# Optimization experiments

Measured on AMD Instinct MI355X. Metric: run time of the kernel, lower is better.

The kernel has to match this reference:

```python
import jax, jax.numpy as jnp
import numpy as np


def gru_layer(x, W_ih, W_hh, b_ih, b_hh):
    """PyTorch-semantics GRU over a full sequence.
    x: [B, T, F]; W_ih: [3H, F]; W_hh: [3H, H]; biases: [3H].
    Gate order (r, z, n) per torch.nn.GRU. Returns [B, T, H].
    """
    B, T, _ = x.shape
    H = W_hh.shape[1]
    # Precompute input projections for all timesteps as one big GEMM: [B, T, 3H]
    xg = jnp.einsum('btf,gf->btg', x, W_ih) + b_ih

    def step(h, xg_t):
        gh = h @ W_hh.T + b_hh                      # [B, 3H]
        xr, xz, xn = jnp.split(xg_t, 3, axis=-1)
        hr, hz, hn = jnp.split(gh, 3, axis=-1)
        r = jax.nn.sigmoid(xr + hr)
        z = jax.nn.sigmoid(xz + hz)
        n = jnp.tanh(xn + r * hn)
        h_new = (1.0 - z) * n + z * h
        return h_new, h_new

    h0 = jnp.zeros((B, H), dtype=x.dtype)
    _, hs = jax.lax.scan(step, h0, jnp.swapaxes(xg, 0, 1))  # hs: [T, B, H]
    return jnp.swapaxes(hs, 0, 1)


def setup_inputs() -> dict:
    key = jax.random.key(0)
    ks = jax.random.split(key, 16)
    B, T, F = 512, 256, 64
    H1, H2, H3 = 256, 128, 64

    def w(k, shape, fan_in):
        s = 1.0 / np.sqrt(fan_in)
        return jax.random.uniform(k, shape, jnp.float32, -s, s)

    return {
        'x': jax.random.normal(ks[0], (B, T, F), jnp.float32),
        'W_ih1': w(ks[1], (3 * H1, F), H1),
        'W_hh1': w(ks[2], (3 * H1, H1), H1),
        'b_ih1': w(ks[3], (3 * H1,), H1),
        'b_hh1': w(ks[4], (3 * H1,), H1),
        'W_ih2': w(ks[5], (3 * H2, H1), H2),
        'W_hh2': w(ks[6], (3 * H2, H2), H2),
        'b_ih2': w(ks[7], (3 * H2,), H2),
        'b_hh2': w(ks[8], (3 * H2,), H2),
        'W_ih3': w(ks[9], (3 * H3, H2), H3),
        'W_hh3': w(ks[10], (3 * H3, H3), H3),
        'b_ih3': w(ks[11], (3 * H3,), H3),
        'b_hh3': w(ks[12], (3 * H3,), H3),
        'W_dense': w(ks[13], (1, H3), H3),
        'b_dense': w(ks[14], (1,), H3),
    }


def reference(x, W_ih1, W_hh1, b_ih1, b_hh1,
              W_ih2, W_hh2, b_ih2, b_hh2,
              W_ih3, W_hh3, b_ih3, b_hh3,
              W_dense, b_dense):
    # Dropout layers act as identity in eval mode.
    h = gru_layer(x, W_ih1, W_hh1, b_ih1, b_hh1)   # [B, T, 256]
    h = gru_layer(h, W_ih2, W_hh2, b_ih2, b_hh2)   # [B, T, 128]
    h = gru_layer(h, W_ih3, W_hh3, b_ih3, b_hh3)   # [B, T, 64]
    last = h[:, -1, :]                              # [B, 64]
    return last @ W_dense.T + b_dense               # [B, 1]
```

## Files before the change

### kernel.cpp

```cpp
#include <hip/hip_runtime.h>
#include <cstddef>

typedef _Float16 f16x8 __attribute__((ext_vector_type(8)));
typedef _Float16 f16x4 __attribute__((ext_vector_type(4)));
typedef short    s16x8 __attribute__((ext_vector_type(8)));
typedef short    s16x4 __attribute__((ext_vector_type(4)));
typedef float    f32x4 __attribute__((ext_vector_type(4)));

#define MFMA_F16(a, b, c) __builtin_amdgcn_mfma_f32_16x16x32_f16((a), (b), (c), 0, 0, 0)

constexpr int GB = 512, GT = 256, GF = 64;
constexpr int H1 = 256, H2 = 128, H3 = 64;

#if __has_builtin(__builtin_amdgcn_rcpf)
__device__ __forceinline__ float fast_rcp(float x) { return __builtin_amdgcn_rcpf(x); }
#else
__device__ __forceinline__ float fast_rcp(float x) { return 1.f / x; }
#endif

__device__ __forceinline__ f16x8 ld8(const short* p) {
  return __builtin_bit_cast(f16x8, *(const s16x8*)p);
}
__device__ __forceinline__ f16x4 ld4(const short* p) {
  return __builtin_bit_cast(f16x4, *(const s16x4*)p);
}

__device__ __forceinline__ void barrier_nodrain() {
  asm volatile("s_waitcnt lgkmcnt(0)" ::: "memory");
  __builtin_amdgcn_s_barrier();
  asm volatile("" ::: "memory");
}

struct CastDesc { const float* src; short* dst; int n; };
struct CastArgs {
  CastDesc d[7];
  const float* bih2; const float* bhh2; float* bc2;
};

__global__ void cast_many(CastArgs a) {
  const int tid = blockIdx.x * blockDim.x + threadIdx.x;
  const int stride = gridDim.x * blockDim.x;
#pragma unroll
  for (int j = 0; j < 7; j++) {
    const float* __restrict__ s = a.d[j].src;
    short* __restrict__ o = a.d[j].dst;
    const int n = a.d[j].n;
    for (int i = tid; i < n; i += stride)
      o[i] = __builtin_bit_cast(short, (_Float16)s[i]);
  }
  for (int i = tid; i < 3 * H2; i += stride)
    a.bc2[i] = a.bih2[i] + (i < 2 * H2 ? a.bhh2[i] : 0.f);
}

template <int K, int NO, int JT>
__device__ __forceinline__ void g_body(const short* __restrict__ A,
                                       const short* __restrict__ W,
                                       const float* __restrict__ biasC,
                                       short* __restrict__ slot, int TC,
                                       int bt, int trel, int tabs, int tid) {
  constexpr int KC = K / 32;
  constexpr int TT = 16;
  const int lane = tid & 63, wid = tid >> 6;
  const int p = lane & 15, q = lane >> 4;
  const int j0 = wid * 16 * JT;

  f16x8 wb[JT][KC];
  float bc[JT];
#pragma unroll
  for (int jt = 0; jt < JT; jt++) {
    const int col = j0 + jt * 16 + p;
    bc[jt] = biasC[col];
#pragma unroll
    for (int kc = 0; kc < KC; kc++)
      wb[jt][kc] = ld8(W + (size_t)col * K + kc * 32 + q * 8);
  }
  const short* arow = A + ((size_t)(bt * 16 + p) * GT + tabs) * K + q * 8;
  short* outb = slot + ((size_t)bt * TC + trel) * NO * 16;

  f16x8 a0[KC], a1[KC];
#pragma unroll
  for (int kc = 0; kc < KC; kc++) a0[kc] = ld8(arow + kc * 32);

  auto step = [&](int ti, f16x8 (&ac)[KC], f16x8 (&anx)[KC], bool pf) {
    if (pf) {
#pragma unroll
      for (int kc = 0; kc < KC; kc++)
        anx[kc] = ld8(arow + (size_t)(ti + 1) * K + kc * 32);
    }
    f32x4 acc[JT];
#pragma unroll
    for (int jt = 0; jt < JT; jt++)
      acc[jt] = f32x4{bc[jt], bc[jt], bc[jt], bc[jt]};
#pragma unroll
    for (int kc = 0; kc < KC; kc++)
#pragma unroll
      for (int jt = 0; jt < JT; jt++)
        acc[jt] = MFMA_F16(ac[kc], wb[jt][kc], acc[jt]);
    short* ob = outb + (size_t)ti * NO * 16;
#pragma unroll
    for (int jt = 0; jt < JT; jt++) {
      const int col = j0 + jt * 16 + p;
      s16x4 v;
#pragma unroll
      for (int r = 0; r < 4; r++)
        v[r] = __builtin_bit_cast(short, (_Float16)acc[jt][r]);
      *(s16x4*)&ob[col * 16 + q * 4] = v;
    }
  };

#pragma unroll 1
  for (int ti = 0; ti < TT; ti += 2) {
    step(ti, a0, a1, true);
    step(ti + 1, a1, a0, ti + 2 < TT);
  }
}

template <int K, int NO, int JT>
__global__ __launch_bounds__(512, 2)
void g_kern(const short* __restrict__ A, const short* __restrict__ W,
            const float* __restrict__ biasC, short* __restrict__ slot,
            int TC, int tbase) {
  const int nty = TC / 16;
  const int bt = blockIdx.x / nty, ty = blockIdx.x - bt * nty;
  g_body<K, NO, JT>(A, W, biasC, slot, TC, bt, ty * 16, tbase + ty * 16, threadIdx.x);
}

__device__ __forceinline__ void r1_run(const short* __restrict__ xg,
                                       const short* __restrict__ Whh,
                                       const float* __restrict__ bhh,
                                       short* __restrict__ hseq,
                                       float* __restrict__ hstate,
                                       int bt, int t0, int t1, int TC,
                                       short* smem, int tid) {
  constexpr int H = H1, KS = H / 32, JT = 2;
  constexpr int HP = H + 8, NO = 3 * H;

  short* wn = smem;
  short* hb = smem + H * HP;

  const int lane = tid & 63, wid = tid >> 6;
  const int p = lane & 15, q = lane >> 4;
  const int b0 = bt * 16, j0 = wid * 16 * JT;

  {
    constexpr int KV = H / 8;
    for (int i = tid; i < H * KV; i += 512) {
      const int row = i / KV, kc = i - row * KV;
      *(s16x8*)&wn[row * HP + kc * 8] =
          *(const s16x8*)&Whh[(size_t)(2 * H + row) * H + kc * 8];
    }
  }
  if (t0 == 0) {
    for (int i = tid; i < 16 * HP; i += 512) hb[i] = 0;
  } else {
    for (int i = tid; i < 16 * H; i += 512) {
      const int row = i / H, col = i - row * H;
      hb[row * HP + col] =
          __builtin_bit_cast(short, (_Float16)hstate[(size_t)(b0 + row) * H + col]);
    }
  }

  f16x8 wr[JT][2][KS];
#pragma unroll
  for (int jt = 0; jt < JT; jt++) {
    const int col = j0 + jt * 16 + p;
#pragma unroll
    for (int g = 0; g < 2; g++)
#pragma unroll
      for (int k = 0; k < KS; k++)
        wr[jt][g][k] = ld8(Whh + (size_t)(g * H + col) * H + k * 32 + q * 8);
  }
  float bhr[JT], bhz[JT], bhn[JT];
  int wrow[JT];
#pragma unroll
  for (int jt = 0; jt < JT; jt++) {
    const int col = j0 + jt * 16 + p;
    wrow[jt] = col;
    bhr[jt] = bhh[col];
    bhz[jt] = bhh[H + col];
    bhn[jt] = bhh[2 * H + col];
  }

  float hprev[JT][4];
#pragma unroll
  for (int jt = 0; jt < JT; jt++)
#pragma unroll
    for (int r = 0; r < 4; r++)
      hprev[jt][r] = (t0 == 0) ? 0.f
                   : hstate[(size_t)(b0 + q * 4 + r) * H + (j0 + jt * 16 + p)];

  const size_t sbase = (size_t)bt * TC * NO * 16;
  int loff[JT][3];
#pragma unroll
  for (int jt = 0; jt < JT; jt++)
#pragma unroll
    for (int g = 0; g < 3; g++)
      loff[jt][g] = (g * H + j0 + jt * 16 + p) * 16 + q * 4;

  f16x4 xb[2][JT][3];
#pragma unroll
  for (int u = 0; u < 2; u++)
#pragma unroll
    for (int jt = 0; jt < JT; jt++)
#pragma unroll
      for (int g = 0; g < 3; g++)
        xb[u][jt][g] = ld4(xg + sbase + (size_t)u * NO * 16 + loff[jt][g]);

  __syncthreads();

  const int steps = t1 - t0;
#pragma unroll 1
  for (int sb = 0; sb < steps; sb += 2) {
#pragma unroll
    for (int u = 0; u < 2; u++) {
      const int s = sb + u, t = t0 + s;
      short* hbc = hb + u * 16 * HP;
      short* hbn = hb + (u ^ 1) * 16 * HP;

      f32x4 ar[JT], az[JT], an[JT];
#pragma unroll
      for (int jt = 0; jt < JT; jt++) {
#pragma unroll
        for (int r = 0; r < 4; r++) {
          ar[jt][r] = (float)xb[u][jt][0][r];
          az[jt][r] = (float)xb[u][jt][1][r];
        }
        an[jt] = f32x4{0.f, 0.f, 0.f, 0.f};
      }
#pragma unroll
      for (int k = 0; k < KS; k++) {
        const f16x8 ahk = ld8(&hbc[p * HP + k * 32 + q * 8]);
#pragma unroll
        for (int jt = 0; jt < JT; jt++) {
          ar[jt] = MFMA_F16(ahk, wr[jt][0][k], ar[jt]);
          az[jt] = MFMA_F16(ahk, wr[jt][1][k], az[jt]);
          const f16x8 wnk = ld8(&wn[wrow[jt] * HP + k * 32 + q * 8]);
          an[jt] = MFMA_F16(ahk, wnk, an[jt]);
        }
      }
#pragma unroll
      for (int jt = 0; jt < JT; jt++) {
        const int col = j0 + jt * 16 + p;
#pragma unroll
        for (int r = 0; r < 4; r++) {
          const int bm = q * 4 + r;
          const float rpre = ar[jt][r] + bhr[jt];
          const float zpre = az[jt][r] + bhz[jt];
          const float rg = fast_rcp(1.f + __expf(-rpre));
          const float zg = fast_rcp(1.f + __expf(-zpre));
          const float narg = (float)xb[u][jt][2][r] + rg * (an[jt][r] + bhn[jt]);
          const float e2 = __expf(2.f * narg);
          const float ng = 1.f - 2.f * fast_rcp(e2 + 1.f);
          const float hnew = (1.f - zg) * ng + zg * hprev[jt][r];
          hprev[jt][r] = hnew;
          const _Float16 hf = (_Float16)hnew;
          hbn[bm * HP + col] = __builtin_bit_cast(short, hf);
          hseq[((size_t)(b0 + bm) * GT + t) * H + col] = __builtin_bit_cast(short, hf);
        }
      }
      if (t == t1 - 1) {
#pragma unroll
        for (int jt = 0; jt < JT; jt++)
#pragma unroll
          for (int r = 0; r < 4; r++)
            hstate[(size_t)(b0 + q * 4 + r) * H + (j0 + jt * 16 + p)] = hprev[jt][r];
      }
      {
        const size_t s2 = sbase + (size_t)(s + 2) * NO * 16;
#pragma unroll
        for (int jt = 0; jt < JT; jt++)
#pragma unroll
          for (int g = 0; g < 3; g++)
            xb[u][jt][g] = ld4(xg + s2 + loff[jt][g]);
      }
      barrier_nodrain();
    }
  }
}

__device__ __forceinline__ void rec23_run(const short* __restrict__ xg2,
                                          const short* __restrict__ Whh2,
                                          const float* __restrict__ bhh2,
                                          const short* __restrict__ Wih3,
                                          const short* __restrict__ Whh3,
                                          const float* __restrict__ bih3,
                                          const float* __restrict__ bhh3,
                                          float* __restrict__ hs2,
                                          float* __restrict__ hs3,
                                          int bt, int t0, int t1, int TC,
                                          short* smem, int tid) {
  constexpr int HP2 = H2 + 8, HP3 = H3 + 8, NO = 3 * H2;
  short* hb2 = smem;
  short* hb3 = smem + 2 * 16 * HP2;

  const int lane = tid & 63, wid = tid >> 6;
  const int p = lane & 15, q = lane >> 4;
  const int b0 = bt * 16;
  const int col2 = wid * 16 + p;
  const int col3 = (wid & 3) * 16 + p;
  const bool act3 = wid < 4;

  if (t0 == 0) {
    for (int i = tid; i < 2 * 16 * HP2; i += 512) hb2[i] = 0;
    for (int i = tid; i < 2 * 16 * HP3; i += 512) hb3[i] = 0;
  } else {
    for (int i = tid; i < 16 * H2; i += 512) {
      const int r = i / H2, c = i - r * H2;
      hb2[r * HP2 + c] = __builtin_bit_cast(short, (_Float16)hs2[(size_t)(b0 + r) * H2 + c]);
    }
    for (int i = tid; i < 16 * H3; i += 512) {
      const int r = i / H3, c = i - r * H3;
      hb3[r * HP3 + c] = __builtin_bit_cast(short, (_Float16)hs3[(size_t)(b0 + r) * H3 + c]);
    }
  }

  f16x8 w2[3][4];
#pragma unroll
  for (int g = 0; g < 3; g++)
#pragma unroll
    for (int k = 0; k < 4; k++)
      w2[g][k] = ld8(Whh2 + (size_t)(g * H2 + col2) * H2 + k * 32 + q * 8);
  const float bn2 = bhh2[2 * H2 + col2];

  f16x8 wi3[3][4], wh3[3][2];
  float br3 = 0.f, bz3 = 0.f, bn3x = 0.f, bn3h = 0.f;
  if (act3) {
#pragma unroll
    for (int g = 0; g < 3; g++) {
#pragma unroll
      for (int k = 0; k < 4; k++)
        wi3[g][k] = ld8(Wih3 + (size_t)(g * H3 + col3) * H2 + k * 32 + q * 8);
#pragma unroll
      for (int k = 0; k < 2; k++)
        wh3[g][k] = ld8(Whh3 + (size_t)(g * H3 + col3) * H3 + k * 32 + q * 8);
    }
    br3 = bih3[col3] + bhh3[col3];
    bz3 = bih3[H3 + col3] + bhh3[H3 + col3];
    bn3x = bih3[2 * H3 + col3];
    bn3h = bhh3[2 * H3 + col3];
  }

  float h2p[4], h3p[4];
#pragma unroll
  for (int r = 0; r < 4; r++) {
    h2p[r] = (t0 == 0) ? 0.f : hs2[(size_t)(b0 + q * 4 + r) * H2 + col2];
    h3p[r] = (!act3 || t0 == 0) ? 0.f : hs3[(size_t)(b0 + q * 4 + r) * H3 + col3];
  }

  const size_t sbase = (size_t)bt * TC * NO * 16;
  int loff[3];
#pragma unroll
  for (int g = 0; g < 3; g++) loff[g] = (g * H2 + col2) * 16 + q * 4;
  f16x4 xb[2][3];
#pragma unroll
  for (int u = 0; u < 2; u++)
#pragma unroll
    for (int g = 0; g < 3; g++)
      xb[u][g] = ld4(xg2 + sbase + (size_t)u * NO * 16 + loff[g]);

  __syncthreads();

  const int steps = t1 - t0;
#pragma unroll 1
  for (int sb = 0; sb < steps; sb += 2) {
#pragma unroll
    for (int u = 0; u < 2; ++u) {
      const int s = sb + u, t = t0 + s;
      f32x4 ar, az, an;
#pragma unroll
      for (int r = 0; r < 4; r++) { ar[r] = (float)xb[u][0][r]; az[r] = (float)xb[u][1][r]; }
      an = f32x4{0.f, 0.f, 0.f, 0.f};
#pragma unroll
      for (int k = 0; k < 4; k++) {
        const f16x8 ahk = ld8(&hb2[(u * 16 + p) * HP2 + k * 32 + q * 8]);
        ar = MFMA_F16(ahk, w2[0][k], ar);
        az = MFMA_F16(ahk, w2[1][k], az);
        an = MFMA_F16(ahk, w2[2][k], an);
      }
#pragma unroll
      for (int r = 0; r < 4; r++) {
        const int bm = q * 4 + r;
        const float rg = fast_rcp(1.f + __expf(-ar[r]));
        const float zg = fast_rcp(1.f + __expf(-az[r]));
        const float narg = (float)xb[u][2][r] + rg * (an[r] + bn2);
        const float e2 = __expf(2.f * narg);
        const float ng = 1.f - 2.f * fast_rcp(e2 + 1.f);
        const float hnew = (1.f - zg) * ng + zg * h2p[r];
        h2p[r] = hnew;
        hb2[((u ^ 1) * 16 + bm) * HP2 + col2] = __builtin_bit_cast(short, (_Float16)hnew);
        if (t == t1 - 1) hs2[(size_t)(b0 + bm) * H2 + col2] = hnew;
      }
      {
        const size_t s2 = sbase + (size_t)(s + 2) * NO * 16;
#pragma unroll
        for (int g = 0; g < 3; g++) xb[u][g] = ld4(xg2 + s2 + loff[g]);
      }
      barrier_nodrain();
      if (act3) {
        f32x4 a3r{0.f,0.f,0.f,0.f}, a3z{0.f,0.f,0.f,0.f},
              a3x{0.f,0.f,0.f,0.f}, a3h{0.f,0.f,0.f,0.f};
#pragma unroll
        for (int k = 0; k < 4; k++) {
          const f16x8 a2k = ld8(&hb2[((u ^ 1) * 16 + p) * HP2 + k * 32 + q * 8]);
          a3r = MFMA_F16(a2k, wi3[0][k], a3r);
          a3z = MFMA_F16(a2k, wi3[1][k], a3z);
          a3x = MFMA_F16(a2k, wi3[2][k], a3x);
        }
#pragma unroll
        for (int k = 0; k < 2; k++) {
          const f16x8 a3k = ld8(&hb3[(u * 16 + p) * HP3 + k * 32 + q * 8]);
          a3r = MFMA_F16(a3k, wh3[0][k], a3r);
          a3z = MFMA_F16(a3k, wh3[1][k], a3z);
          a3h = MFMA_F16(a3k, wh3[2][k], a3h);
        }
#pragma unroll
        for (int r = 0; r < 4; r++) {
          const int bm = q * 4 + r;
          const float rg = fast_rcp(1.f + __expf(-(a3r[r] + br3)));
          const float zg = fast_rcp(1.f + __expf(-(a3z[r] + bz3)));
          const float narg = a3x[r] + bn3x + rg * (a3h[r] + bn3h);
          const float e2 = __expf(2.f * narg);
          const float ng = 1.f - 2.f * fast_rcp(e2 + 1.f);
          const float hnew = (1.f - zg) * ng + zg * h3p[r];
          h3p[r] = hnew;
          hb3[((u ^ 1) * 16 + bm) * HP3 + col3] = __builtin_bit_cast(short, (_Float16)hnew);
          if (t == t1 - 1) hs3[(size_t)(b0 + bm) * H3 + col3] = hnew;
        }
      }
    }
  }
}

__global__ __launch_bounds__(512, 2)
void fused1(const short* __restrict__ xg_rd, short* __restrict__ xg_wr,
            const short* __restrict__ xh, const short* __restrict__ wih1,
            const float* __restrict__ bih1, const short* __restrict__ whh1,
            const float* __restrict__ bhh1, short* __restrict__ h1,
            float* __restrict__ hs1, int t0, int TC) {
  extern __shared__ __align__(16) short smem[];
  if (blockIdx.x < 32) {
    r1_run(xg_rd, whh1, bhh1, h1, hs1, blockIdx.x, t0, t0 + TC, TC, smem, threadIdx.x);
  } else if (xg_wr) {
    const int g = blockIdx.x - 32, nty = TC / 16;
    const int bt = g / nty, ty = g - bt * nty;
    g_body<GF, 3 * H1, 6>(xh, wih1, bih1, xg_wr, TC, bt, ty * 16,
                          t0 + TC + ty * 16, threadIdx.x);
  }
}

__global__ __launch_bounds__(512, 2)
void fused2(const short* __restrict__ xg_rd, short* __restrict__ xg_wr,
            const short* __restrict__ h1, const short* __restrict__ wih2,
            const float* __restrict__ bc2, const short* __restrict__ whh2,
            const float* __restrict__ bhh2, const short* __restrict__ wih3,
            const short* __restrict__ whh3, const float* __restrict__ bih3,
            const float* __restrict__ bhh3, float* __restrict__ hs2,
            float* __restrict__ hs3, int t0, int TC) {
  extern __shared__ __align__(16) short smem[];
  if (blockIdx.x < 32) {
    rec23_run(xg_rd, whh2, bhh2, wih3, whh3, bih3, bhh3, hs2, hs3,
              blockIdx.x, t0, t0 + TC, TC, smem, threadIdx.x);
  } else if (xg_wr) {
    const int g = blockIdx.x - 32, nty = TC / 16;
    const int bt = g / nty, ty = g - bt * nty;
    g_body<H1, 3 * H2, 3>(h1, wih2, bc2, xg_wr, TC, bt, ty * 16,
                          t0 + TC + ty * 16, threadIdx.x);
  }
}

__global__ void dense_kernel(const float* __restrict__ hl, const float* __restrict__ Wd,
                             const float* __restrict__ bd, float* __restrict__ out) {
  const int b = blockIdx.x * 64 + threadIdx.x;
  float a = bd[0];
#pragma unroll
  for (int k = 0; k < 64; k++) a = fmaf(hl[b * 64 + k], Wd[k], a);
  out[b] = a;
}

extern "C" void kernel_launch(void* const* d_in, const int* in_sizes, int n_in,
                              void* d_out, int out_size, void* d_ws, size_t ws_size,
                              hipStream_t stream) {
  constexpr int B = GB, T = GT, F = GF;
  constexpr int M = B * T;

  const float* x     = (const float*)d_in[0];
  const float* W_ih1 = (const float*)d_in[1];
  const float* W_hh1 = (const float*)d_in[2];
  const float* b_ih1 = (const float*)d_in[3];
  const float* b_hh1 = (const float*)d_in[4];
  const float* W_ih2 = (const float*)d_in[5];
  const float* W_hh2 = (const float*)d_in[6];
  const float* b_ih2 = (const float*)d_in[7];
  const float* b_hh2 = (const float*)d_in[8];
  const float* W_ih3 = (const float*)d_in[9];
  const float* W_hh3 = (const float*)d_in[10];
  const float* b_ih3 = (const float*)d_in[11];
  const float* b_hh3 = (const float*)d_in[12];
  const float* W_d   = (const float*)d_in[13];
  const float* b_d   = (const float*)d_in[14];
  float* out = (float*)d_out;

  char* ws = (char*)d_ws;
  size_t off = 0;
  auto alloc = [&](size_t bytes) -> char* {
    char* pp = ws + off;
    off = (off + bytes + 255) & ~(size_t)255;
    return pp;
  };

  const int nx    = M * F;
  const int nwih1 = 3 * H1 * F,  nwhh1 = 3 * H1 * H1;
  const int nwih2 = 3 * H2 * H1, nwhh2 = 3 * H2 * H2;
  const int nwih3 = 3 * H3 * H2, nwhh3 = 3 * H3 * H3;

  short* xh   = (short*)alloc((size_t)nx * 2);
  short* wih1 = (short*)alloc((size_t)nwih1 * 2);
  short* whh1 = (short*)alloc((size_t)nwhh1 * 2);
  short* wih2 = (short*)alloc((size_t)nwih2 * 2);
  short* whh2 = (short*)alloc((size_t)nwhh2 * 2);
  short* wih3 = (short*)alloc((size_t)nwih3 * 2);
  short* whh3 = (short*)alloc((size_t)nwhh3 * 2);
  short* h1   = (short*)alloc((size_t)M * H1 * 2);
  float* hs1  = (float*)alloc((size_t)B * H1 * 4);
  float* hs2  = (float*)alloc((size_t)B * H2 * 4);
  float* hs3  = (float*)alloc((size_t)B * H3 * 4);
  float* bc2  = (float*)alloc(3 * H2 * 4);
  (void)n_in; (void)in_sizes; (void)out_size;

  const size_t avail = (ws_size > off) ? (ws_size - off) : 0;
  int TC = 64;
  auto need = [&](int tc) -> size_t {
    return 2 * ((size_t)32 * tc * (3 * H1) * 16 * 2)
         + 2 * ((size_t)32 * tc * (3 * H2) * 16 * 2) + 2 * 65536;
  };
  while (TC > 16 && need(TC) > avail) TC >>= 1;
  const int NC = T / TC, nty = TC / 16;
  const size_t slot1e = (size_t)32 * TC * (3 * H1) * 16;
  const size_t slot2e = (size_t)32 * TC * (3 * H2) * 16;
  short* ring1 = (short*)alloc(2 * slot1e * 2 + 65536);
  short* ring2 = (short*)alloc(2 * slot2e * 2 + 65536);

  CastArgs ca;
  ca.d[0] = {x, xh, nx};
  ca.d[1] = {W_ih1, wih1, nwih1};
  ca.d[2] = {W_hh1, whh1, nwhh1};
  ca.d[3] = {W_ih2, wih2, nwih2};
  ca.d[4] = {W_hh2, whh2, nwhh2};
  ca.d[5] = {W_ih3, wih3, nwih3};
  ca.d[6] = {W_hh3, whh3, nwhh3};
  ca.bih2 = b_ih2; ca.bhh2 = b_hh2; ca.bc2 = bc2;
  cast_many<<<1024, 256, 0, stream>>>(ca);

  constexpr int SM1 = H1 * (H1 + 8) * 2 + 2 * 16 * (H1 + 8) * 2;
  constexpr int SM2 = 2 * 16 * (H2 + 8) * 2 + 2 * 16 * (H3 + 8) * 2;
  (void)hipFuncSetAttribute((const void*)fused1,
                            hipFuncAttributeMaxDynamicSharedMemorySize, SM1);

  g_kern<GF, 3 * H1, 6><<<32 * nty, 512, 0, stream>>>(xh, wih1, b_ih1, ring1, TC, 0);
  for (int c = 0; c < NC; ++c) {
    const short* rd = ring1 + (size_t)(c & 1) * slot1e;
    short* wr = (c + 1 < NC) ? ring1 + (size_t)((c + 1) & 1) * slot1e : nullptr;
    fused1<<<32 + (wr ? 32 * nty : 0), 512, SM1, stream>>>(
        rd, wr, xh, wih1, b_ih1, whh1, b_hh1, h1, hs1, c * TC, TC);
  }
  g_kern<H1, 3 * H2, 3><<<32 * nty, 512, 0, stream>>>(h1, wih2, bc2, ring2, TC, 0);
  for (int c = 0; c < NC; ++c) {
    const short* rd = ring2 + (size_t)(c & 1) * slot2e;
    short* wr = (c + 1 < NC) ? ring2 + (size_t)((c + 1) & 1) * slot2e : nullptr;
    fused2<<<32 + (wr ? 32 * nty : 0), 512, SM2, stream>>>(
        rd, wr, h1, wih2, bc2, whh2, b_hh2, wih3, whh3, b_ih3, b_hh3,
        hs2, hs3, c * TC, TC);
  }

  dense_kernel<<<B / 64, 64, 0, stream>>>(hs3, W_d, b_d, out);
}
```

Measured before the change: 940.0 us.

## Wavefront-pipeline layer-1 and layer-2/3 recurrences across time chunks in one kernel

Merges the two per-layer chunk loops into a single launch sequence. Each launch runs the layer-1 recurrence on chunk c and the fused layer-2/3 recurrence on chunk c-2 at the same time. In the same launch, other blocks compute the layer-1 input projection for chunk c+1 and the layer-2 input projection for chunk c-1. This lets the two serial recurrences overlap instead of running back to back, and removes the separate layer-2 prologue GEMM. In exchange every block requests the larger layer-1 shared-memory size, which may lower occupancy. The recurrence blocks also now share the GPU with more concurrent work.

```diff
diff --git a/kernel.cpp b/kernel.cpp
--- a/kernel.cpp
+++ b/kernel.cpp
@@ -431,40 +431,48 @@
   }
 }
 
+struct PipeArgs {
+  const short* xh;
+  const short* wih1; const short* whh1; const float* bih1; const float* bhh1;
+  const short* wih2; const float* bc2;  const short* whh2; const float* bhh2;
+  const short* wih3; const short* whh3; const float* bih3; const float* bhh3;
+  short* h1; float* hs1; float* hs2; float* hs3;
+  short* ring1; short* ring2;
+  size_t slot1e, slot2e;
+  int c, NC, TC;
+};
+
 __global__ __launch_bounds__(512, 2)
-void fused1(const short* __restrict__ xg_rd, short* __restrict__ xg_wr,
-            const short* __restrict__ xh, const short* __restrict__ wih1,
-            const float* __restrict__ bih1, const short* __restrict__ whh1,
-            const float* __restrict__ bhh1, short* __restrict__ h1,
-            float* __restrict__ hs1, int t0, int TC) {
+void fused_all(PipeArgs a) {
   extern __shared__ __align__(16) short smem[];
-  if (blockIdx.x < 32) {
-    r1_run(xg_rd, whh1, bhh1, h1, hs1, blockIdx.x, t0, t0 + TC, TC, smem, threadIdx.x);
-  } else if (xg_wr) {
-    const int g = blockIdx.x - 32, nty = TC / 16;
-    const int bt = g / nty, ty = g - bt * nty;
-    g_body<GF, 3 * H1, 6>(xh, wih1, bih1, xg_wr, TC, bt, ty * 16,
-                          t0 + TC + ty * 16, threadIdx.x);
-  }
-}
-
-__global__ __launch_bounds__(512, 2)
-void fused2(const short* __restrict__ xg_rd, short* __restrict__ xg_wr,
-            const short* __restrict__ h1, const short* __restrict__ wih2,
-            const float* __restrict__ bc2, const short* __restrict__ whh2,
-            const float* __restrict__ bhh2, const short* __restrict__ wih3,
-            const short* __restrict__ whh3, const float* __restrict__ bih3,
-            const float* __restrict__ bhh3, float* __restrict__ hs2,
-            float* __restrict__ hs3, int t0, int TC) {
-  extern __shared__ __align__(16) short smem[];
-  if (blockIdx.x < 32) {
-    rec23_run(xg_rd, whh2, bhh2, wih3, whh3, bih3, bhh3, hs2, hs3,
-              blockIdx.x, t0, t0 + TC, TC, smem, threadIdx.x);
-  } else if (xg_wr) {
-    const int g = blockIdx.x - 32, nty = TC / 16;
-    const int bt = g / nty, ty = g - bt * nty;
-    g_body<H1, 3 * H2, 3>(h1, wih2, bc2, xg_wr, TC, bt, ty * 16,
-                          t0 + TC + ty * 16, threadIdx.x);
+  const int nty = a.TC / 16, GW = 32 * nty;
+  const int bid = blockIdx.x, tid = threadIdx.x;
+  if (bid < 32) {
+    if (a.c < a.NC)
+      r1_run(a.ring1 + (size_t)(a.c & 1) * a.slot1e, a.whh1, a.bhh1, a.h1, a.hs1,
+             bid, a.c * a.TC, (a.c + 1) * a.TC, a.TC, smem, tid);
+  } else if (bid < 64) {
+    const int cc = a.c - 2;
+    if (cc >= 0 && cc < a.NC)
+      rec23_run(a.ring2 + (size_t)(cc & 1) * a.slot2e, a.whh2, a.bhh2,
+                a.wih3, a.whh3, a.bih3, a.bhh3, a.hs2, a.hs3,
+                bid - 32, cc * a.TC, (cc + 1) * a.TC, a.TC, smem, tid);
+  } else if (bid < 64 + GW) {
+    const int cc = a.c + 1;
+    if (cc < a.NC) {
+      const int g = bid - 64, bt = g / nty, ty = g - bt * nty;
+      g_body<GF, 3 * H1, 6>(a.xh, a.wih1, a.bih1,
+                            a.ring1 + (size_t)(cc & 1) * a.slot1e, a.TC,
+                            bt, ty * 16, cc * a.TC + ty * 16, tid);
+    }
+  } else {
+    const int cc = a.c - 1;
+    if (cc >= 0 && cc < a.NC) {
+      const int g = bid - 64 - GW, bt = g / nty, ty = g - bt * nty;
+      g_body<H1, 3 * H2, 3>(a.h1, a.wih2, a.bc2,
+                            a.ring2 + (size_t)(cc & 1) * a.slot2e, a.TC,
+                            bt, ty * 16, cc * a.TC + ty * 16, tid);
+    }
   }
 }
 
@@ -552,24 +560,25 @@
   cast_many<<<1024, 256, 0, stream>>>(ca);
 
   constexpr int SM1 = H1 * (H1 + 8) * 2 + 2 * 16 * (H1 + 8) * 2;
-  constexpr int SM2 = 2 * 16 * (H2 + 8) * 2 + 2 * 16 * (H3 + 8) * 2;
-  (void)hipFuncSetAttribute((const void*)fused1,
+  (void)hipFuncSetAttribute((const void*)fused_all,
                             hipFuncAttributeMaxDynamicSharedMemorySize, SM1);
 
   g_kern<GF, 3 * H1, 6><<<32 * nty, 512, 0, stream>>>(xh, wih1, b_ih1, ring1, TC, 0);
-  for (int c = 0; c < NC; ++c) {
-    const short* rd = ring1 + (size_t)(c & 1) * slot1e;
-    short* wr = (c + 1 < NC) ? ring1 + (size_t)((c + 1) & 1) * slot1e : nullptr;
-    fused1<<<32 + (wr ? 32 * nty : 0), 512, SM1, stream>>>(
-        rd, wr, xh, wih1, b_ih1, whh1, b_hh1, h1, hs1, c * TC, TC);
-  }
-  g_kern<H1, 3 * H2, 3><<<32 * nty, 512, 0, stream>>>(h1, wih2, bc2, ring2, TC, 0);
-  for (int c = 0; c < NC; ++c) {
-    const short* rd = ring2 + (size_t)(c & 1) * slot2e;
-    short* wr = (c + 1 < NC) ? ring2 + (size_t)((c + 1) & 1) * slot2e : nullptr;
-    fused2<<<32 + (wr ? 32 * nty : 0), 512, SM2, stream>>>(
-        rd, wr, h1, wih2, bc2, whh2, b_hh2, wih3, whh3, b_ih3, b_hh3,
-        hs2, hs3, c * TC, TC);
+
+  PipeArgs pa;
+  pa.xh = xh;
+  pa.wih1 = wih1; pa.whh1 = whh1; pa.bih1 = b_ih1; pa.bhh1 = b_hh1;
+  pa.wih2 = wih2; pa.bc2 = bc2;   pa.whh2 = whh2; pa.bhh2 = b_hh2;
+  pa.wih3 = wih3; pa.whh3 = whh3; pa.bih3 = b_ih3; pa.bhh3 = b_hh3;
+  pa.h1 = h1; pa.hs1 = hs1; pa.hs2 = hs2; pa.hs3 = hs3;
+  pa.ring1 = ring1; pa.ring2 = ring2;
+  pa.slot1e = slot1e; pa.slot2e = slot2e;
+  pa.NC = NC; pa.TC = TC;
+
+  const int grid = 64 + 2 * (32 * nty);
+  for (int c = 0; c <= NC + 1; ++c) {
+    pa.c = c;
+    fused_all<<<grid, 512, SM1, stream>>>(pa);
   }
 
   dense_kernel<<<B / 64, 64, 0, stream>>>(hs3, W_d, b_d, out);
```

After: 767.1 us. -18.4%, faster.
